# Kernel optimization log

Hardware: AMD Instinct MI355X
Metric: run time of the kernel (lower is better)

The kernel has to match this reference:

```python
import jax, jax.numpy as jnp
import numpy as np

NV, NG, D, K, NB = 4096, 2048, 64, 128, 4
C_IN, C_OUT, E = 128, 8, 32768
SIGMA = 2.5  # rbf sigma used in the non-mp path


def _gcn_conv(x, src, dst, w, b, n):
    # PyG GCNConv (edge_weight=None, self loops already appended to src/dst)
    deg = jax.ops.segment_sum(jnp.ones(src.shape, x.dtype), dst, num_segments=n)
    dinv = jnp.where(deg > 0, 1.0 / jnp.sqrt(deg), 0.0)
    norm = dinv[src] * dinv[dst]
    h = x @ w
    return jax.ops.segment_sum(h[src] * norm[:, None], dst, num_segments=n) + b


def _diff_block(x, mass, evals, evecs, gradX, gradY, t, a_re, a_im, w0, b0, w1, b1, w2, b2):
    # learned-time spectral diffusion
    x_spec = evecs.T @ (x * mass[:, None])                      # [K, D]
    coef = jnp.exp(-evals[:, None] * jnp.clip(t, 1e-8)[None, :])  # [K, D]
    x_diff = evecs @ (coef * x_spec)                            # [NV, D]
    # spatial gradient features: complex grad, learned rotation, tanh of inner product
    gX = gradX @ x_diff                                         # real part  [NV, D]
    gY = gradY @ x_diff                                         # imag part  [NV, D]
    b_re = gX @ a_re - gY @ a_im
    b_im = gY @ a_re + gX @ a_im
    gfeat = jnp.tanh(gX * b_re + gY * b_im)
    f = jnp.concatenate([x, x_diff, gfeat], axis=-1)            # [NV, 3D]
    h = jax.nn.relu(f @ w0 + b0)
    h = jax.nn.relu(h @ w1 + b1)
    return h @ w2 + b2 + x                                      # residual skip


def _forward(surf_x, mass, evals, evecs, gradX, gradY, vertices, graph_x, graph_pos,
             lin1_w, lin1_b, lin2_w, lin2_b, last_w, last_b,
             diff_time, A_re, A_im, mlp_w0, mlp_b0, mlp_w1, mlp_b1, mlp_w2, mlp_b2,
             gcn_w1, gcn_b1, gcn_w2, gcn_b2, edge_index):
    nv, ng = vertices.shape[0], graph_pos.shape[0]
    # dense rbf coupling (torch.no_grad in original -> stop_gradient)
    d2 = (jnp.sum(vertices * vertices, 1)[:, None]
          + jnp.sum(graph_pos * graph_pos, 1)[None, :]
          - 2.0 * (vertices @ graph_pos.T))
    dist = jnp.sqrt(jnp.clip(d2, 0.0))
    rbf = jax.lax.stop_gradient(jnp.exp(-dist / SIGMA))          # [NV, NG]
    diff_x = surf_x @ lin1_w + lin1_b                            # [NV, D]
    gx = graph_x @ lin2_w + lin2_b                               # [NG, D]
    loops = jnp.arange(ng, dtype=edge_index.dtype)
    src = jnp.concatenate([edge_index[0], loops])
    dst = jnp.concatenate([edge_index[1], loops])
    for i in range(NB):
        diff_x = _diff_block(diff_x, mass, evals, evecs, gradX, gradY,
                             diff_time[i], A_re[i], A_im[i],
                             mlp_w0[i], mlp_b0[i], mlp_w1[i], mlp_b1[i], mlp_w2[i], mlp_b2[i])
        gx = rbf.T @ diff_x                                      # surface -> graph
        h = jax.nn.relu(_gcn_conv(gx, src, dst, gcn_w1[i], gcn_b1[i], ng))
        gx = _gcn_conv(h, src, dst, gcn_w2[i], gcn_b2[i], ng)
        diff_x = rbf @ gx                                        # graph -> surface
    return diff_x @ last_w + last_b                              # [NV, C_OUT]


def setup_inputs() -> dict:
    key = jax.random.key(0)
    ks = jax.random.split(key, 24)
    f32 = jnp.float32
    def rn(k, shape, scale=1.0):
        return jax.random.normal(k, shape, f32) * scale
    inp = {
        'surf_x': rn(ks[0], (NV, 5)),
        'mass': jax.random.uniform(ks[1], (NV,), f32, 0.1, 1.0),
        'evals': jnp.sort(jax.random.uniform(ks[2], (K,), f32, 0.0, 50.0)),
        'evecs': rn(ks[3], (NV, K), 1.0 / np.sqrt(NV)),
        'gradX': rn(ks[4], (NV, NV), 1.0 / np.sqrt(NV)),
        'gradY': rn(ks[5], (NV, NV), 1.0 / np.sqrt(NV)),
        'vertices': rn(ks[6], (NV, 3), 5.0),
        'graph_x': rn(ks[7], (NG, C_IN)),
        'graph_pos': rn(ks[8], (NG, 3), 5.0),
        'lin1_w': rn(ks[9], (5, D), 1.0 / np.sqrt(5)),
        'lin1_b': jnp.zeros((D,), f32),
        'lin2_w': rn(ks[10], (C_IN, D), 1.0 / np.sqrt(C_IN)),
        'lin2_b': jnp.zeros((D,), f32),
        'last_w': rn(ks[11], (D, C_OUT), 1.0 / np.sqrt(D)),
        'last_b': jnp.zeros((C_OUT,), f32),
        'diff_time': jax.random.uniform(ks[12], (NB, D), f32, 1e-3, 1.0),
        'A_re': rn(ks[13], (NB, D, D), 1.0 / np.sqrt(D)),
        'A_im': rn(ks[14], (NB, D, D), 1.0 / np.sqrt(D)),
        'mlp_w0': rn(ks[15], (NB, 3 * D, D), 1.0 / np.sqrt(3 * D)),
        'mlp_b0': jnp.zeros((NB, D), f32),
        'mlp_w1': rn(ks[16], (NB, D, D), 1.0 / np.sqrt(D)),
        'mlp_b1': jnp.zeros((NB, D), f32),
        'mlp_w2': rn(ks[17], (NB, D, D), 1.0 / np.sqrt(D)),
        'mlp_b2': jnp.zeros((NB, D), f32),
        'gcn_w1': rn(ks[18], (NB, D, D), 1.0 / np.sqrt(D)),
        'gcn_b1': jnp.zeros((NB, D), f32),
        'gcn_w2': rn(ks[19], (NB, D, D), 1.0 / np.sqrt(D)),
        'gcn_b2': jnp.zeros((NB, D), f32),
        'edge_index': jax.random.randint(ks[20], (2, E), 0, NG, dtype=jnp.int32),
    }
    return inp


def reference(surf_x, mass, evals, evecs, gradX, gradY, vertices, graph_x, graph_pos,
              lin1_w, lin1_b, lin2_w, lin2_b, last_w, last_b,
              diff_time, A_re, A_im, mlp_w0, mlp_b0, mlp_w1, mlp_b1, mlp_w2, mlp_b2,
              gcn_w1, gcn_b1, gcn_w2, gcn_b2, edge_index):
    return _forward(surf_x, mass, evals, evecs, gradX, gradY, vertices, graph_x, graph_pos,
                    lin1_w, lin1_b, lin2_w, lin2_b, last_w, last_b,
                    diff_time, A_re, A_im, mlp_w0, mlp_b0, mlp_w1, mlp_b1, mlp_w2, mlp_b2,
                    gcn_w1, gcn_b1, gcn_w2, gcn_b2, edge_index)
```

## Files before the change

kernel.cpp:

```cpp
#include <hip/hip_runtime.h>
#include <hip/hip_bf16.h>

#define NVV 4096
#define NGG 2048
#define DD 64
#define KSP 128
#define NBLK 4
#define NEDGE 32768
#define COUT 8
#define NSLICE_G 16
#define NSLICE_V 8
#define NSLICE_S 32
#define VS 32
#define GXE_KSL 16

typedef __hip_bfloat16 bf16;
using bf16x8 = __attribute__((ext_vector_type(8))) __bf16;
using s16x8  = __attribute__((ext_vector_type(8))) short;
using f32x4  = __attribute__((ext_vector_type(4))) float;

__device__ __forceinline__ float toF(bf16 x){ return __bfloat162float(x); }
__device__ __forceinline__ float ldin(const void* p, size_t i, int f){
  return f ? toF(((const bf16*)p)[i]) : ((const float*)p)[i];
}
__device__ __forceinline__ short f2bf(float x){
  __bf16 b = (__bf16)x;
  return __builtin_bit_cast(short, b);
}
__device__ __forceinline__ float bf2f(short s){
  return (float)__builtin_bit_cast(__bf16, s);
}
__device__ __forceinline__ bf16x8 ld8(const short* p){
  return __builtin_bit_cast(bf16x8, *(const s16x8*)p);
}
__device__ __forceinline__ void gl16(const short* g, short* l){
  __builtin_amdgcn_global_load_lds((__attribute__((address_space(1))) void*)(g),
                                   (__attribute__((address_space(3))) void*)(l),
                                   16, 0, 0);
}

__global__ void k_probe(const void* __restrict__ mass, int* __restrict__ flag){
  int t = threadIdx.x;
  float v = toF(((const bf16*)mass)[t]);
  bool ok = (v >= 0.05f) && (v <= 1.05f);
  unsigned long long m = __ballot(ok);
  if (t == 0) flag[0] = (m == ~0ull) ? 1 : 0;
}

__global__ void k_csr_zero(int* c){ int g = blockIdx.x*256+threadIdx.x; if (g<NGG) c[g]=0; }
__global__ void k_csr_cnt(const int* __restrict__ ei, int* __restrict__ c){
  int e = blockIdx.x*256+threadIdx.x; if (e<NEDGE) atomicAdd(&c[ei[NEDGE+e]], 1);
}
__global__ void k_csr_scan(const int* __restrict__ cnt, int* __restrict__ off,
                           int* __restrict__ cursor, float* __restrict__ dinv){
  __shared__ int ws[256];
  int t = threadIdx.x;
  int base = t*8;
  int local[8]; int s = 0;
  #pragma unroll
  for (int i=0;i<8;i++){ local[i]=s; s += cnt[base+i]; }
  ws[t] = s;
  __syncthreads();
  for (int o=1;o<256;o<<=1){
    int v = (t>=o) ? ws[t-o] : 0;
    __syncthreads();
    ws[t] += v;
    __syncthreads();
  }
  int pre = (t==0) ? 0 : ws[t-1];
  #pragma unroll
  for (int i=0;i<8;i++){
    int o = pre + local[i];
    off[base+i] = o; cursor[base+i] = o;
    dinv[base+i] = rsqrtf(1.f + (float)cnt[base+i]);
  }
  if (t==255) off[NGG] = pre + s;
}
__global__ void k_csr_fill(const int* __restrict__ ei, int* __restrict__ cursor,
                           int* __restrict__ csrc){
  int e = blockIdx.x*256+threadIdx.x;
  if (e < NEDGE){
    int d = ei[NEDGE+e];
    int p = atomicAdd(&cursor[d], 1);
    csrc[p] = ei[e];
  }
}

__global__ void k_lin1_mx(const void* __restrict__ sx, const void* __restrict__ w,
                          const void* __restrict__ b, const void* __restrict__ mass,
                          float* __restrict__ out, short* __restrict__ btMX,
                          const int* __restrict__ flg){
  const int f = *flg;
  __shared__ short tl[64*68];
  const int t = threadIdx.x;
  const int r = t>>2, c0 = (t&3)*16;
  const size_t v = (size_t)blockIdx.x*64 + r;
  float sxa[5];
  #pragma unroll
  for (int k=0;k<5;k++) sxa[k] = ldin(sx, v*5+k, f);
  const float mv = ldin(mass, v, f);
  float acc[16];
  #pragma unroll
  for (int j=0;j<16;j++){
    float a = ldin(b, c0+j, f);
    #pragma unroll
    for (int k=0;k<5;k++) a += sxa[k]*ldin(w, (size_t)k*DD + c0 + j, f);
    acc[j] = a;
    tl[(size_t)(c0+j)*68 + r] = f2bf(a*mv);
  }
  float* op = out + v*DD + c0;
  ((float4*)op)[0] = *(float4*)&acc[0];
  ((float4*)op)[1] = *(float4*)&acc[4];
  ((float4*)op)[2] = *(float4*)&acc[8];
  ((float4*)op)[3] = *(float4*)&acc[12];
  __syncthreads();
  s16x8 u0, u1;
  #pragma unroll
  for (int j=0;j<8;j++){ u0[j]=tl[(size_t)r*68+c0+j]; u1[j]=tl[(size_t)r*68+c0+8+j]; }
  const int s8 = (r&7)<<3;
  short* dp = btMX + (size_t)blockIdx.x*4096 + (size_t)r*64;
  *(s16x8*)&dp[c0 ^ s8]     = u0;
  *(s16x8*)&dp[(c0+8) ^ s8] = u1;
}

__global__ void k_spec_red(const float* __restrict__ partial, const void* __restrict__ evals,
                           const void* __restrict__ tvec, int boff,
                           short* __restrict__ btA, const int* __restrict__ flg){
  const int f = *flg;
  int idx = blockIdx.x*256 + threadIdx.x;
  int k = idx >> 6, d = idx & 63;
  float sum = 0.f;
  #pragma unroll 8
  for (int s = 0; s < VS; s++) sum += partial[(size_t)s*KSP*DD + idx];
  float t = fmaxf(ldin(tvec, boff + d, f), 1e-8f);
  float val = expf(-ldin(evals, k, f) * t) * sum;
  btA[(size_t)(k>>6)*4096 + (size_t)d*64 + ((k&63) ^ ((d&7)<<3))] = f2bf(val);
}

__global__ void k_cvt_a(const void* __restrict__ src, short* __restrict__ dst,
                        int Kfull, const int* __restrict__ flg){
  const int f = *flg;
  const int t = threadIdx.x;
  const int r = t>>2, c0 = (t&3)*16;
  const size_t row = (size_t)blockIdx.x*64 + r;
  const size_t base = row*(size_t)Kfull + (size_t)blockIdx.y*64 + c0;
  s16x8 v0, v1;
  if (f){
    const short* sp = (const short*)src + base;
    v0 = ((const s16x8*)sp)[0];
    v1 = ((const s16x8*)sp)[1];
  } else {
    const float* sp = (const float*)src + base;
    float tmp[16];
    ((float4*)tmp)[0] = ((const float4*)sp)[0];
    ((float4*)tmp)[1] = ((const float4*)sp)[1];
    ((float4*)tmp)[2] = ((const float4*)sp)[2];
    ((float4*)tmp)[3] = ((const float4*)sp)[3];
    #pragma unroll
    for (int i=0;i<8;i++){ v0[i]=f2bf(tmp[i]); v1[i]=f2bf(tmp[8+i]); }
  }
  const int s8 = (r&7)<<3;
  short* dp = dst + ((size_t)blockIdx.x*(Kfull>>6) + blockIdx.y)*4096 + (size_t)r*64;
  *(s16x8*)&dp[c0 ^ s8]     = v0;
  *(s16x8*)&dp[(c0+8) ^ s8] = v1;
}

__global__ void k_cvt_at(const void* __restrict__ evecs, short* __restrict__ dst,
                         const int* __restrict__ flg){
  const int f = *flg;
  __shared__ short tl[64*68];
  const int t = threadIdx.x;
  const int r = t>>2, c0 = (t&3)*16;
  const int kt = blockIdx.x, s = blockIdx.y;
  const size_t v = (size_t)kt*64 + r;
  #pragma unroll
  for (int j=0;j<16;j++)
    tl[(size_t)(c0+j)*68 + r] = f2bf(ldin(evecs, v*KSP + (size_t)s*64 + c0 + j, f));
  __syncthreads();
  s16x8 u0, u1;
  #pragma unroll
  for (int j=0;j<8;j++){ u0[j]=tl[(size_t)r*68+c0+j]; u1[j]=tl[(size_t)r*68+c0+8+j]; }
  const int s8 = (r&7)<<3;
  short* dp = dst + ((size_t)s*64 + kt)*4096 + (size_t)r*64;
  *(s16x8*)&dp[c0 ^ s8]     = u0;
  *(s16x8*)&dp[(c0+8) ^ s8] = u1;
}

__global__ void k_rbf_pre(const void* __restrict__ P, const void* __restrict__ Q,
                          short* __restrict__ rbfV, short* __restrict__ rbfG,
                          const int* __restrict__ flg){
  const int f = *flg;
  __shared__ short tl[64*68];
  const int t = threadIdx.x;
  const int r = t>>2, c0 = (t&3)*16;
  const int vt = blockIdx.x, gt = blockIdx.y;
  const float px = ldin(P, ((size_t)vt*64+r)*3+0, f);
  const float py = ldin(P, ((size_t)vt*64+r)*3+1, f);
  const float pz = ldin(P, ((size_t)vt*64+r)*3+2, f);
  s16x8 v0, v1;
  #pragma unroll
  for (int j=0;j<16;j++){
    const size_t g = (size_t)gt*64 + c0 + j;
    float dx = px - ldin(Q, g*3+0, f);
    float dy = py - ldin(Q, g*3+1, f);
    float dz = pz - ldin(Q, g*3+2, f);
    short s = f2bf(__expf(-sqrtf(dx*dx+dy*dy+dz*dz)*0.4f));
    if (j<8) v0[j] = s; else v1[j-8] = s;
    tl[(size_t)(c0+j)*68 + r] = s;
  }
  const int s8 = (r&7)<<3;
  short* vp = rbfV + ((size_t)vt*(NGG/64) + gt)*4096 + (size_t)r*64;
  *(s16x8*)&vp[c0 ^ s8]     = v0;
  *(s16x8*)&vp[(c0+8) ^ s8] = v1;
  __syncthreads();
  s16x8 u0, u1;
  #pragma unroll
  for (int j=0;j<8;j++){ u0[j] = tl[(size_t)r*68 + c0 + j]; u1[j] = tl[(size_t)r*68 + c0 + 8 + j]; }
  short* gp = rbfG + ((size_t)gt*(NVV/64) + vt)*4096 + (size_t)r*64;
  *(s16x8*)&gp[c0 ^ s8]     = u0;
  *(s16x8*)&gp[(c0+8) ^ s8] = u1;
}

__global__ void k_cvt_wt(const void* __restrict__ Are, const void* __restrict__ Aim,
                         const void* __restrict__ w0, const void* __restrict__ w1,
                         const void* __restrict__ w2,
                         short* __restrict__ btRe, short* __restrict__ btIm,
                         short* __restrict__ btW0, short* __restrict__ btW1,
                         short* __restrict__ btW2, const int* __restrict__ flg){
  const int f = *flg;
  __shared__ short tl[64*68];
  const int t = threadIdx.x;
  const int r = t>>2, c0 = (t&3)*16;
  const int slot = blockIdx.x, b = blockIdx.y;
  const void* src; size_t soff; short* dst; float scale = 1.f;
  switch(slot){
    case 0: src=Are; soff=(size_t)b*4096; dst=btRe + (size_t)b*2*4096;               break;
    case 1: src=Aim; soff=(size_t)b*4096; dst=btRe + (size_t)b*2*4096 + 4096; scale=-1.f; break;
    case 2: src=Aim; soff=(size_t)b*4096; dst=btIm + (size_t)b*2*4096;               break;
    case 3: src=Are; soff=(size_t)b*4096; dst=btIm + (size_t)b*2*4096 + 4096;        break;
    case 4: case 5: case 6:
      src=w0; soff=(size_t)b*3*4096 + (size_t)(slot-4)*4096;
      dst=btW0 + (size_t)b*3*4096 + (size_t)(slot-4)*4096;                           break;
    case 7: src=w1; soff=(size_t)b*4096; dst=btW1 + (size_t)b*4096;                  break;
    default: src=w2; soff=(size_t)b*4096; dst=btW2 + (size_t)b*4096;                 break;
  }
  #pragma unroll
  for (int j=0;j<16;j++)
    tl[(size_t)(c0+j)*68 + r] = f2bf(scale * ldin(src, soff + (size_t)r*64 + c0 + j, f));
  __syncthreads();
  s16x8 u0, u1;
  #pragma unroll
  for (int j=0;j<8;j++){ u0[j]=tl[(size_t)r*68+c0+j]; u1[j]=tl[(size_t)r*68+c0+8+j]; }
  const int s8 = (r&7)<<3;
  short* dp = dst + (size_t)r*64;
  *(s16x8*)&dp[c0 ^ s8]     = u0;
  *(s16x8*)&dp[(c0+8) ^ s8] = u1;
}

template<int TWO>
__global__ void k_gemm_pre(const short* __restrict__ A0, const short* __restrict__ A1,
                           const short* __restrict__ Bt, float* __restrict__ C,
                           int M, int ktt, int tps, int yoff, short* __restrict__ btOut){
  constexpr int NBUF = TWO ? 3 : 2;
  __shared__ __align__(16) short sm[2*NBUF*4096];
  const int t = threadIdx.x;
  const int w = t>>6, lane = t&63;
  const int fr = lane&15, fq = lane>>4;
  const int strip = blockIdx.x, sl = blockIdx.y;
  const size_t abase = ((size_t)strip*ktt + (size_t)sl*tps)*4096;
  const short* gA0 = A0 + abase;
  const short* gA1 = TWO ? (A1 + abase) : A0;
  const short* gB  = Bt + (size_t)sl*tps*4096;
  const int to = t*8;

  auto stage = [&](int p, int kt){
    short* l = &sm[p*NBUF*4096];
    const size_t ko = (size_t)kt*4096;
    gl16(gA0 + ko + to,        l + (w<<9));
    gl16(gA0 + ko + 2048 + to, l + 2048 + (w<<9));
    if (TWO){
      gl16(gA1 + ko + to,        l + 4096 + (w<<9));
      gl16(gA1 + ko + 2048 + to, l + 6144 + (w<<9));
    }
    short* lb = l + (TWO ? 8192 : 4096);
    gl16(gB + ko + to,        lb + (w<<9));
    gl16(gB + ko + 2048 + to, lb + 2048 + (w<<9));
  };

  f32x4 acc0[4] = {{0,0,0,0},{0,0,0,0},{0,0,0,0},{0,0,0,0}};
  f32x4 acc1[4] = {{0,0,0,0},{0,0,0,0},{0,0,0,0},{0,0,0,0}};

  stage(0, 0);
  int cur = 0;
  const int arow = w*16 + fr;
  const int ax0 = arow*64;
  const int asw = (arow&7)<<3;
  for (int kt=0; kt<tps; ++kt){
    if (kt+1 < tps){
      stage(cur^1, kt+1);
      if constexpr (TWO) asm volatile("s_waitcnt vmcnt(6)" ::: "memory");
      else               asm volatile("s_waitcnt vmcnt(4)" ::: "memory");
    } else {
      asm volatile("s_waitcnt vmcnt(0)" ::: "memory");
    }
    __builtin_amdgcn_s_barrier();
    asm volatile("" ::: "memory");
    const short* As  = &sm[cur*NBUF*4096];
    const short* A1s = As + 4096;
    const short* Bs  = As + (TWO ? 8192 : 4096);
    #pragma unroll
    for (int ks=0; ks<2; ks++){
      const int kx = ks*32 + fq*8;
      bf16x8 a0 = ld8(&As[ax0 + (kx ^ asw)]);
      bf16x8 a1 = TWO ? ld8(&A1s[ax0 + (kx ^ asw)]) : a0;
      #pragma unroll
      for (int nc=0;nc<4;nc++){
        const int brow = nc*16 + fr;
        bf16x8 b = ld8(&Bs[brow*64 + (kx ^ ((brow&7)<<3))]);
        acc0[nc] = __builtin_amdgcn_mfma_f32_16x16x32_bf16(a0, b, acc0[nc], 0, 0, 0);
        if constexpr (TWO)
          acc1[nc] = __builtin_amdgcn_mfma_f32_16x16x32_bf16(a1, b, acc1[nc], 0, 0, 0);
      }
    }
    asm volatile("" ::: "memory");
    __builtin_amdgcn_s_barrier();
    cur ^= 1;
  }
  float* C0 = C + (size_t)sl*M*DD;
  const int row0 = strip*64 + w*16 + fq*4;
  #pragma unroll
  for (int nc=0;nc<4;nc++)
    #pragma unroll
    for (int r=0;r<4;r++)
      C0[(size_t)(row0+r)*DD + nc*16 + fr] = acc0[nc][r];
  if constexpr (TWO){
    float* C1 = C + (size_t)yoff + (size_t)sl*M*DD;
    #pragma unroll
    for (int nc=0;nc<4;nc++)
      #pragma unroll
      for (int r=0;r<4;r++)
        C1[(size_t)(row0+r)*DD + nc*16 + fr] = acc1[nc][r];
  }
  if (btOut){
    #pragma unroll
    for (int nc=0;nc<4;nc++)
      #pragma unroll
      for (int r=0;r<4;r++){
        int k = row0 + r, n = nc*16 + fr;
        btOut[(size_t)(k>>6)*4096 + (size_t)n*64 + ((k&63) ^ ((n&7)<<3))] = f2bf(acc0[nc][r]);
      }
  }
}

__global__ void k_gxe_raw(const void* __restrict__ gradX, const void* __restrict__ gradY,
                          const short* __restrict__ evsT, float* __restrict__ part,
                          const int* __restrict__ flg){
  const int f = *flg;
  __shared__ __align__(16) short sm[4*4096];
  const int t = threadIdx.x;
  const int w = t>>6, lane = t&63;
  const int fr = lane&15, fq = lane>>4;
  const int strip = blockIdx.x, ksl = blockIdx.y;
  const int sr = t>>2, sc = (t&3)*16;
  const int to = t*8;
  const int arow = w*16 + fr;
  const int asw = (arow&7)<<3;
  const int s8 = (sr&7)<<3;
  f32x4 aX0[4] = {{0,0,0,0},{0,0,0,0},{0,0,0,0},{0,0,0,0}};
  f32x4 aX1[4] = {{0,0,0,0},{0,0,0,0},{0,0,0,0},{0,0,0,0}};
  f32x4 aY0[4] = {{0,0,0,0},{0,0,0,0},{0,0,0,0},{0,0,0,0}};
  f32x4 aY1[4] = {{0,0,0,0},{0,0,0,0},{0,0,0,0},{0,0,0,0}};
  for (int kt=0; kt<4; ++kt){
    const int ktg = ksl*4 + kt;
    const size_t abase = ((size_t)strip*64 + sr)*NVV + (size_t)ktg*64 + sc;
    s16x8 x0, x1, y0, y1;
    if (f==0){
      const float* ax = (const float*)gradX + abase;
      const float* ay = (const float*)gradY + abase;
      float bx[16], by[16];
      ((float4*)bx)[0]=((const float4*)ax)[0]; ((float4*)bx)[1]=((const float4*)ax)[1];
      ((float4*)bx)[2]=((const float4*)ax)[2]; ((float4*)bx)[3]=((const float4*)ax)[3];
      ((float4*)by)[0]=((const float4*)ay)[0]; ((float4*)by)[1]=((const float4*)ay)[1];
      ((float4*)by)[2]=((const float4*)ay)[2]; ((float4*)by)[3]=((const float4*)ay)[3];
      #pragma unroll
      for (int j=0;j<8;j++){ x0[j]=f2bf(bx[j]); x1[j]=f2bf(bx[8+j]);
                             y0[j]=f2bf(by[j]); y1[j]=f2bf(by[8+j]); }
    } else {
      const short* ax = (const short*)gradX + abase;
      const short* ay = (const short*)gradY + abase;
      x0 = ((const s16x8*)ax)[0]; x1 = ((const s16x8*)ax)[1];
      y0 = ((const s16x8*)ay)[0]; y1 = ((const s16x8*)ay)[1];
    }
    *(s16x8*)&sm[0*4096 + sr*64 + (sc ^ s8)]     = x0;
    *(s16x8*)&sm[0*4096 + sr*64 + ((sc+8) ^ s8)] = x1;
    *(s16x8*)&sm[1*4096 + sr*64 + (sc ^ s8)]     = y0;
    *(s16x8*)&sm[1*4096 + sr*64 + ((sc+8) ^ s8)] = y1;
    gl16(evsT + (size_t)ktg*4096 + to,             &sm[2*4096] + (w<<9));
    gl16(evsT + (size_t)ktg*4096 + 2048 + to,      &sm[2*4096] + 2048 + (w<<9));
    gl16(evsT + (size_t)(64+ktg)*4096 + to,        &sm[3*4096] + (w<<9));
    gl16(evsT + (size_t)(64+ktg)*4096 + 2048 + to, &sm[3*4096] + 2048 + (w<<9));
    __syncthreads();
    #pragma unroll
    for (int ks=0; ks<2; ks++){
      const int kx = ks*32 + fq*8;
      bf16x8 aXv = ld8(&sm[0*4096 + arow*64 + (kx ^ asw)]);
      bf16x8 aYv = ld8(&sm[1*4096 + arow*64 + (kx ^ asw)]);
      #pragma unroll
      for (int nc=0;nc<4;nc++){
        const int brow = nc*16 + fr, bsw = (brow&7)<<3;
        bf16x8 b0 = ld8(&sm[2*4096 + brow*64 + (kx ^ bsw)]);
        bf16x8 b1 = ld8(&sm[3*4096 + brow*64 + (kx ^ bsw)]);
        aX0[nc] = __builtin_amdgcn_mfma_f32_16x16x32_bf16(aXv, b0, aX0[nc], 0, 0, 0);
        aX1[nc] = __builtin_amdgcn_mfma_f32_16x16x32_bf16(aXv, b1, aX1[nc], 0, 0, 0);
        aY0[nc] = __builtin_amdgcn_mfma_f32_16x16x32_bf16(aYv, b0, aY0[nc], 0, 0, 0);
        aY1[nc] = __builtin_amdgcn_mfma_f32_16x16x32_bf16(aYv, b1, aY1[nc], 0, 0, 0);
      }
    }
    __syncthreads();
  }
  const int row0 = strip*64 + w*16 + fq*4;
  float* C0 = part + (size_t)(ksl)*NVV*DD;
  float* C1 = part + (size_t)(GXE_KSL+ksl)*NVV*DD;
  float* C2 = part + (size_t)(2*GXE_KSL+ksl)*NVV*DD;
  float* C3 = part + (size_t)(3*GXE_KSL+ksl)*NVV*DD;
  #pragma unroll
  for (int nc=0;nc<4;nc++)
    #pragma unroll
    for (int r=0;r<4;r++){
      const size_t o = (size_t)(row0+r)*DD + nc*16 + fr;
      C0[o] = aX0[nc][r];
      C1[o] = aX1[nc][r];
      C2[o] = aY0[nc][r];
      C3[o] = aY1[nc][r];
    }
}

__global__ void k_fold_at(const float* __restrict__ part, short* __restrict__ dX,
                          short* __restrict__ dY){
  const int t = threadIdx.x;
  const int r = t>>2, c0 = (t&3)*16;
  const int strip = blockIdx.x, s = blockIdx.y;
  float ax[16], ay[16];
  #pragma unroll
  for (int j=0;j<16;j++){ ax[j]=0.f; ay[j]=0.f; }
  const float* pb = part + ((size_t)strip*64 + r)*DD + c0;
  for (int sl=0; sl<GXE_KSL; sl++){
    const float* px = pb + (size_t)(s*GXE_KSL+sl)*NVV*DD;
    const float* py = pb + (size_t)(2*GXE_KSL+s*GXE_KSL+sl)*NVV*DD;
    #pragma unroll
    for (int q=0;q<4;q++){
      float4 a = ((const float4*)px)[q];
      float4 b = ((const float4*)py)[q];
      ax[q*4+0]+=a.x; ax[q*4+1]+=a.y; ax[q*4+2]+=a.z; ax[q*4+3]+=a.w;
      ay[q*4+0]+=b.x; ay[q*4+1]+=b.y; ay[q*4+2]+=b.z; ay[q*4+3]+=b.w;
    }
  }
  s16x8 x0,x1,y0,y1;
  #pragma unroll
  for (int j=0;j<8;j++){ x0[j]=f2bf(ax[j]); x1[j]=f2bf(ax[8+j]);
                         y0[j]=f2bf(ay[j]); y1[j]=f2bf(ay[8+j]); }
  const int s8 = (r&7)<<3;
  short* dpx = dX + ((size_t)strip*2 + s)*4096 + (size_t)r*64;
  short* dpy = dY + ((size_t)strip*2 + s)*4096 + (size_t)r*64;
  *(s16x8*)&dpx[c0 ^ s8]     = x0;
  *(s16x8*)&dpx[(c0+8) ^ s8] = x1;
  *(s16x8*)&dpy[c0 ^ s8]     = y0;
  *(s16x8*)&dpy[(c0+8) ^ s8] = y1;
}

__global__ void k_reduce_mx(const float* __restrict__ P, const void* __restrict__ mass,
                            float* __restrict__ C, short* __restrict__ btMX,
                            int slices, const int* __restrict__ flg){
  const int f = *flg;
  __shared__ short tl[64*68];
  const int t = threadIdx.x;
  const int r = t>>2, c0 = (t&3)*16;
  const size_t v = (size_t)blockIdx.x*64 + r;
  float acc[16];
  #pragma unroll
  for (int j=0;j<16;j++) acc[j] = 0.f;
  const float* pb = P + v*DD + c0;
  for (int s=0;s<slices;s++){
    const float* ps = pb + (size_t)s*NVV*DD;
    #pragma unroll
    for (int q=0;q<4;q++){
      float4 a = ((const float4*)ps)[q];
      acc[q*4+0]+=a.x; acc[q*4+1]+=a.y; acc[q*4+2]+=a.z; acc[q*4+3]+=a.w;
    }
  }
  float* op = C + v*DD + c0;
  ((float4*)op)[0] = *(float4*)&acc[0];
  ((float4*)op)[1] = *(float4*)&acc[4];
  ((float4*)op)[2] = *(float4*)&acc[8];
  ((float4*)op)[3] = *(float4*)&acc[12];
  const float mv = ldin(mass, v, f);
  #pragma unroll
  for (int j=0;j<16;j++) tl[(size_t)(c0+j)*68 + r] = f2bf(acc[j]*mv);
  __syncthreads();
  s16x8 u0, u1;
  #pragma unroll
  for (int j=0;j<8;j++){ u0[j]=tl[(size_t)r*68+c0+j]; u1[j]=tl[(size_t)r*68+c0+8+j]; }
  const int s8 = (r&7)<<3;
  short* dp = btMX + (size_t)blockIdx.x*4096 + (size_t)r*64;
  *(s16x8*)&dp[c0 ^ s8]     = u0;
  *(s16x8*)&dp[(c0+8) ^ s8] = u1;
}

__global__ void k_tail_fused(const short* __restrict__ evsA, const short* __restrict__ GXE,
                             const short* __restrict__ GYE, const short* __restrict__ btA,
                             const float* __restrict__ cur,
                             const short* __restrict__ btRe, const short* __restrict__ btIm,
                             const short* __restrict__ btW0, const short* __restrict__ btW1,
                             const short* __restrict__ btW2,
                             const void* __restrict__ b0, const void* __restrict__ b1,
                             const void* __restrict__ b2, int boff,
                             short* __restrict__ btOut, const int* __restrict__ flg){
  __shared__ __align__(16) short sm[8*4096];
  const int f = *flg;
  const int t = threadIdx.x;
  const int w = t>>6, lane = t&63;
  const int fr = lane&15, fq = lane>>4;
  const int strip = blockIdx.x;
  const int to = t*8;
  const int arow = w*16 + fr;
  const int asw = (arow&7)<<3;
  #pragma unroll
  for (int kt=0; kt<2; kt++){
    const size_t ko = ((size_t)strip*2 + kt)*4096;
    gl16(evsA + ko + to,        &sm[kt*4096] + (w<<9));
    gl16(evsA + ko + 2048 + to, &sm[kt*4096] + 2048 + (w<<9));
    gl16(GXE + ko + to,         &sm[(2+kt)*4096] + (w<<9));
    gl16(GXE + ko + 2048 + to,  &sm[(2+kt)*4096] + 2048 + (w<<9));
    gl16(GYE + ko + to,         &sm[(4+kt)*4096] + (w<<9));
    gl16(GYE + ko + 2048 + to,  &sm[(4+kt)*4096] + 2048 + (w<<9));
    gl16(btA + (size_t)kt*4096 + to,        &sm[(6+kt)*4096] + (w<<9));
    gl16(btA + (size_t)kt*4096 + 2048 + to, &sm[(6+kt)*4096] + 2048 + (w<<9));
  }
  __syncthreads();
  f32x4 aX[4]  = {{0,0,0,0},{0,0,0,0},{0,0,0,0},{0,0,0,0}};
  f32x4 aGX[4] = {{0,0,0,0},{0,0,0,0},{0,0,0,0},{0,0,0,0}};
  f32x4 aGY[4] = {{0,0,0,0},{0,0,0,0},{0,0,0,0},{0,0,0,0}};
  #pragma unroll
  for (int kt=0; kt<2; kt++){
    const short* Ae = &sm[kt*4096];
    const short* Ax = &sm[(2+kt)*4096];
    const short* Ay = &sm[(4+kt)*4096];
    const short* Bs = &sm[(6+kt)*4096];
    #pragma unroll
    for (int ks=0; ks<2; ks++){
      const int kx = ks*32 + fq*8;
      bf16x8 ae = ld8(&Ae[arow*64 + (kx ^ asw)]);
      bf16x8 ax = ld8(&Ax[arow*64 + (kx ^ asw)]);
      bf16x8 ay = ld8(&Ay[arow*64 + (kx ^ asw)]);
      #pragma unroll
      for (int nc=0;nc<4;nc++){
        const int brow = nc*16 + fr;
        bf16x8 b = ld8(&Bs[brow*64 + (kx ^ ((brow&7)<<3))]);
        aX[nc]  = __builtin_amdgcn_mfma_f32_16x16x32_bf16(ae, b, aX[nc], 0, 0, 0);
        aGX[nc] = __builtin_amdgcn_mfma_f32_16x16x32_bf16(ax, b, aGX[nc], 0, 0, 0);
        aGY[nc] = __builtin_amdgcn_mfma_f32_16x16x32_bf16(ay, b, aGY[nc], 0, 0, 0);
      }
    }
  }
  __syncthreads();
  gl16(btRe + to,        &sm[2*4096] + (w<<9));
  gl16(btRe + 2048 + to, &sm[2*4096] + 2048 + (w<<9));
  gl16(btRe + 4096 + to, &sm[3*4096] + (w<<9));
  gl16(btRe + 6144 + to, &sm[3*4096] + 2048 + (w<<9));
  gl16(btIm + to,        &sm[4*4096] + (w<<9));
  gl16(btIm + 2048 + to, &sm[4*4096] + 2048 + (w<<9));
  gl16(btIm + 4096 + to, &sm[5*4096] + (w<<9));
  gl16(btIm + 6144 + to, &sm[5*4096] + 2048 + (w<<9));
  #pragma unroll
  for (int nc=0;nc<4;nc++)
    #pragma unroll
    for (int r2=0;r2<4;r2++){
      const int mi = w*16 + fq*4 + r2, n = nc*16 + fr;
      const int pos = mi*64 + (n ^ ((mi&7)<<3));
      sm[0*4096 + pos] = f2bf(aGX[nc][r2]);
      sm[1*4096 + pos] = f2bf(aGY[nc][r2]);
      sm[7*4096 + pos] = f2bf(aX[nc][r2]);
    }
  {
    const int r = t>>2, c0 = (t&3)*16;
    const float* cp = cur + ((size_t)strip*64 + r)*DD + c0;
    float ca[16];
    ((float4*)ca)[0]=((const float4*)cp)[0]; ((float4*)ca)[1]=((const float4*)cp)[1];
    ((float4*)ca)[2]=((const float4*)cp)[2]; ((float4*)ca)[3]=((const float4*)cp)[3];
    s16x8 v0,v1;
    #pragma unroll
    for (int j=0;j<8;j++){ v0[j]=f2bf(ca[j]); v1[j]=f2bf(ca[8+j]); }
    const int s8 = (r&7)<<3;
    *(s16x8*)&sm[6*4096 + r*64 + (c0 ^ s8)]     = v0;
    *(s16x8*)&sm[6*4096 + r*64 + ((c0+8) ^ s8)] = v1;
  }
  __syncthreads();
  f32x4 re[4] = {{0,0,0,0},{0,0,0,0},{0,0,0,0},{0,0,0,0}};
  f32x4 im[4] = {{0,0,0,0},{0,0,0,0},{0,0,0,0},{0,0,0,0}};
  #pragma unroll
  for (int kt=0; kt<2; kt++){
    const short* As = &sm[kt*4096];
    const short* Br = &sm[(2+kt)*4096];
    const short* Bi = &sm[(4+kt)*4096];
    #pragma unroll
    for (int ks=0; ks<2; ks++){
      const int kx = ks*32 + fq*8;
      bf16x8 a = ld8(&As[arow*64 + (kx ^ asw)]);
      #pragma unroll
      for (int nc=0;nc<4;nc++){
        const int brow = nc*16 + fr, bsw = (brow&7)<<3;
        bf16x8 br_ = ld8(&Br[brow*64 + (kx ^ bsw)]);
        bf16x8 bi_ = ld8(&Bi[brow*64 + (kx ^ bsw)]);
        re[nc] = __builtin_amdgcn_mfma_f32_16x16x32_bf16(a, br_, re[nc], 0, 0, 0);
        im[nc] = __builtin_amdgcn_mfma_f32_16x16x32_bf16(a, bi_, im[nc], 0, 0, 0);
      }
    }
  }
  __syncthreads();
  gl16(btW0 + to,           &sm[2*4096] + (w<<9));
  gl16(btW0 + 2048 + to,    &sm[2*4096] + 2048 + (w<<9));
  gl16(btW0 + 4096 + to,    &sm[3*4096] + (w<<9));
  gl16(btW0 + 6144 + to,    &sm[3*4096] + 2048 + (w<<9));
  gl16(btW0 + 8192 + to,    &sm[4*4096] + (w<<9));
  gl16(btW0 + 10240 + to,   &sm[4*4096] + 2048 + (w<<9));
  gl16(btW1 + to,           &sm[5*4096] + (w<<9));
  gl16(btW1 + 2048 + to,    &sm[5*4096] + 2048 + (w<<9));
  float gfv[4][4];
  #pragma unroll
  for (int nc=0;nc<4;nc++){
    const int n = nc*16 + fr;
    #pragma unroll
    for (int r2=0;r2<4;r2++){
      const int mi = w*16 + fq*4 + r2;
      const int pos = mi*64 + (n ^ ((mi&7)<<3));
      float gx = bf2f(sm[pos]);
      float gy = bf2f(sm[4096 + pos]);
      gfv[nc][r2] = tanhf(gx*re[nc][r2] + gy*im[nc][r2]);
    }
  }
  __syncthreads();
  gl16(btW2 + to,        &sm[1*4096] + (w<<9));
  gl16(btW2 + 2048 + to, &sm[1*4096] + 2048 + (w<<9));
  #pragma unroll
  for (int nc=0;nc<4;nc++)
    #pragma unroll
    for (int r2=0;r2<4;r2++){
      const int mi = w*16 + fq*4 + r2, n = nc*16 + fr;
      sm[mi*64 + (n ^ ((mi&7)<<3))] = f2bf(gfv[nc][r2]);
    }
  __syncthreads();
  f32x4 acc[4] = {{0,0,0,0},{0,0,0,0},{0,0,0,0},{0,0,0,0}};
  #pragma unroll
  for (int kt=0; kt<3; kt++){
    const short* As = &sm[(kt==0 ? 6 : (kt==1 ? 7 : 0))*4096];
    const short* Bs = &sm[(2+kt)*4096];
    #pragma unroll
    for (int ks=0; ks<2; ks++){
      const int kx = ks*32 + fq*8;
      bf16x8 a = ld8(&As[arow*64 + (kx ^ asw)]);
      #pragma unroll
      for (int nc=0;nc<4;nc++){
        const int brow = nc*16 + fr;
        bf16x8 b = ld8(&Bs[brow*64 + (kx ^ ((brow&7)<<3))]);
        acc[nc] = __builtin_amdgcn_mfma_f32_16x16x32_bf16(a, b, acc[nc], 0, 0, 0);
      }
    }
  }
  __syncthreads();
  #pragma unroll
  for (int nc=0;nc<4;nc++){
    float bz = ldin(b0, boff + nc*16 + fr, f);
    #pragma unroll
    for (int r2=0;r2<4;r2++){
      const int mi = w*16 + fq*4 + r2, n = nc*16 + fr;
      sm[6*4096 + mi*64 + (n ^ ((mi&7)<<3))] = f2bf(fmaxf(acc[nc][r2] + bz, 0.f));
    }
  }
  __syncthreads();
  f32x4 a1c[4] = {{0,0,0,0},{0,0,0,0},{0,0,0,0},{0,0,0,0}};
  #pragma unroll
  for (int ks=0; ks<2; ks++){
    const int kx = ks*32 + fq*8;
    bf16x8 a = ld8(&sm[6*4096 + arow*64 + (kx ^ asw)]);
    #pragma unroll
    for (int nc=0;nc<4;nc++){
      const int brow = nc*16 + fr;
      bf16x8 b = ld8(&sm[5*4096 + brow*64 + (kx ^ ((brow&7)<<3))]);
      a1c[nc] = __builtin_amdgcn_mfma_f32_16x16x32_bf16(a, b, a1c[nc], 0, 0, 0);
    }
  }
  #pragma unroll
  for (int nc=0;nc<4;nc++){
    float bz = ldin(b1, boff + nc*16 + fr, f);
    #pragma unroll
    for (int r2=0;r2<4;r2++){
      const int mi = w*16 + fq*4 + r2, n = nc*16 + fr;
      sm[7*4096 + mi*64 + (n ^ ((mi&7)<<3))] = f2bf(fmaxf(a1c[nc][r2] + bz, 0.f));
    }
  }
  __syncthreads();
  f32x4 a2c[4] = {{0,0,0,0},{0,0,0,0},{0,0,0,0},{0,0,0,0}};
  #pragma unroll
  for (int ks=0; ks<2; ks++){
    const int kx = ks*32 + fq*8;
    bf16x8 a = ld8(&sm[7*4096 + arow*64 + (kx ^ asw)]);
    #pragma unroll
    for (int nc=0;nc<4;nc++){
      const int brow = nc*16 + fr;
      bf16x8 b = ld8(&sm[1*4096 + brow*64 + (kx ^ ((brow&7)<<3))]);
      a2c[nc] = __builtin_amdgcn_mfma_f32_16x16x32_bf16(a, b, a2c[nc], 0, 0, 0);
    }
  }
  const int row0 = strip*64 + w*16 + fq*4;
  #pragma unroll
  for (int nc=0;nc<4;nc++){
    float bz = ldin(b2, boff + nc*16 + fr, f);
    #pragma unroll
    for (int r2=0;r2<4;r2++){
      int row = row0 + r2, n = nc*16 + fr;
      float vv = a2c[nc][r2] + bz + cur[(size_t)row*DD + n];
      btOut[(size_t)(row>>6)*4096 + (size_t)n*64 + ((row&63) ^ ((n&7)<<3))] = f2bf(vv);
    }
  }
}

__global__ void k_gcn1(const float* __restrict__ part, const void* __restrict__ W,
                       int woff, const float* __restrict__ dinv,
                       const void* __restrict__ bias, int boff,
                       float* __restrict__ tmp, float* __restrict__ outinit,
                       const int* __restrict__ flg){
  const int f = *flg;
  __shared__ float xs[4][DD];
  int d = threadIdx.x & 63, vl = threadIdx.x >> 6;
  size_t g = (size_t)blockIdx.x*4 + vl;
  float x = 0.f;
  #pragma unroll
  for (int s = 0; s < NSLICE_G; s++) x += part[(size_t)s*NGG*DD + g*DD + d];
  xs[vl][d] = x;
  __syncthreads();
  float acc = 0.f;
  #pragma unroll 8
  for (int k=0;k<DD;k++) acc += xs[vl][k]*ldin(W, (size_t)woff + k*DD + d, f);
  tmp[g*DD+d] = acc;
  float di = dinv[g];
  outinit[g*DD+d] = acc*di*di + ldin(bias, boff + d, f);
}

__global__ void k_gcn2f(const float* __restrict__ selfinit, const float* __restrict__ tmp,
                        const int* __restrict__ off, const int* __restrict__ csrc,
                        const float* __restrict__ dinv, const void* __restrict__ W,
                        int woff, const void* __restrict__ bias, int boff,
                        float* __restrict__ tmp2, float* __restrict__ out2init,
                        const int* __restrict__ flg){
  const int f = *flg;
  __shared__ float xs[4][DD];
  int d = threadIdx.x & 63, vl = threadIdx.x >> 6;
  size_t g = (size_t)blockIdx.x*4 + vl;
  float dg = dinv[g];
  float agg = selfinit[g*DD+d];
  int s1 = off[g+1];
  for (int i = off[g]; i < s1; i++){
    int sv = csrc[i];
    agg += tmp[(size_t)sv*DD+d]*(dinv[sv]*dg);
  }
  xs[vl][d] = fmaxf(agg, 0.f);
  __syncthreads();
  float acc = 0.f;
  #pragma unroll 8
  for (int k=0;k<DD;k++) acc += xs[vl][k]*ldin(W, (size_t)woff + k*DD + d, f);
  tmp2[g*DD+d] = acc;
  out2init[g*DD+d] = acc*dg*dg + ldin(bias, boff + d, f);
}

__global__ void k_aggr_t(const float* __restrict__ selfinit, const float* __restrict__ tmp,
                         const int* __restrict__ off, const int* __restrict__ csrc,
                         const float* __restrict__ dinv, short* __restrict__ dst){
  __shared__ short tl[64*68];
  const int t = threadIdx.x;
  const int r = t>>2, c0 = (t&3)*16;
  const size_t g = (size_t)blockIdx.x*64 + r;
  const float dg = dinv[g];
  float agg[16];
  const float* sp = selfinit + g*DD + c0;
  ((float4*)agg)[0] = ((const float4*)sp)[0];
  ((float4*)agg)[1] = ((const float4*)sp)[1];
  ((float4*)agg)[2] = ((const float4*)sp)[2];
  ((float4*)agg)[3] = ((const float4*)sp)[3];
  const int e1 = off[g+1];
  for (int i = off[g]; i < e1; i++){
    const int sv = csrc[i];
    const float w_ = dinv[sv]*dg;
    const float* tp = tmp + (size_t)sv*DD + c0;
    #pragma unroll
    for (int q=0;q<4;q++){
      float4 a = ((const float4*)tp)[q];
      agg[q*4+0]+=a.x*w_; agg[q*4+1]+=a.y*w_; agg[q*4+2]+=a.z*w_; agg[q*4+3]+=a.w*w_;
    }
  }
  #pragma unroll
  for (int j=0;j<16;j++) tl[(size_t)(c0+j)*68 + r] = f2bf(agg[j]);
  __syncthreads();
  s16x8 u0,u1;
  #pragma unroll
  for (int j=0;j<8;j++){ u0[j]=tl[(size_t)r*68+c0+j]; u1[j]=tl[(size_t)r*68+c0+8+j]; }
  const int s8 = (r&7)<<3;
  short* dp = dst + (size_t)blockIdx.x*4096 + (size_t)r*64;
  *(s16x8*)&dp[c0 ^ s8]     = u0;
  *(s16x8*)&dp[(c0+8) ^ s8] = u1;
}

__global__ void k_final(const float* __restrict__ x, const void* __restrict__ w,
                        const void* __restrict__ b, void* __restrict__ outv,
                        const int* __restrict__ flg){
  const int f = *flg;
  int idx = blockIdx.x*256 + threadIdx.x;
  int v = idx >> 3, c = idx & 7;
  float acc = ldin(b, c, f);
  #pragma unroll 8
  for (int k=0;k<DD;k++) acc += x[(size_t)v*DD+k]*ldin(w, (size_t)k*COUT+c, f);
  if (f) ((bf16*)outv)[idx] = __float2bfloat16(acc);
  else   ((float*)outv)[idx] = acc;
}

extern "C" void kernel_launch(void* const* d_in, const int* in_sizes, int n_in,
                              void* d_out, int out_size, void* d_ws, size_t ws_size,
                              hipStream_t stream){
  (void)in_sizes; (void)n_in;
  const void* surf_x   = d_in[0];
  const void* mass     = d_in[1];
  const void* evals    = d_in[2];
  const void* evecs    = d_in[3];
  const void* gradX    = d_in[4];
  const void* gradY    = d_in[5];
  const void* vertices = d_in[6];
  const void* gpos     = d_in[8];
  const void* lin1_w   = d_in[9];
  const void* lin1_b   = d_in[10];
  const void* last_w   = d_in[13];
  const void* last_b   = d_in[14];
  const void* dtime    = d_in[15];
  const void* A_re     = d_in[16];
  const void* A_im     = d_in[17];
  const void* mw0      = d_in[18];
  const void* mb0      = d_in[19];
  const void* mw1      = d_in[20];
  const void* mb1      = d_in[21];
  const void* mw2      = d_in[22];
  const void* mb2      = d_in[23];
  const void* gw1      = d_in[24];
  const void* gb1      = d_in[25];
  const void* gw2      = d_in[26];
  const void* gb2      = d_in[27];
  const int*  ei       = (const int*)d_in[28];

  const size_t REQUIRED = (size_t)115*1024*1024;
  if (ws_size < REQUIRED){
    hipMemsetAsync(d_out, 0, (size_t)out_size*2, stream);
    return;
  }
  char* p = (char*)d_ws;
  auto alloc = [&](size_t bytes)->void*{
    void* r = (void*)p;
    p += (bytes + 255) & ~(size_t)255;
    return r;
  };
  float* part  = (float*)alloc((size_t)64*NVV*DD*4);
  float* bufA  = (float*)alloc((size_t)NVV*DD*4);
  float* tmpg  = (float*)alloc((size_t)NGG*DD*4);
  float* hg    = (float*)alloc((size_t)NGG*DD*4);
  float* tmp2  = (float*)alloc((size_t)NGG*DD*4);
  float* o2    = (float*)alloc((size_t)NGG*DD*4);
  float* dinv  = (float*)alloc((size_t)NGG*4);
  int*   flg   = (int*)alloc(256);
  int*   cnt   = (int*)alloc((size_t)NGG*4);
  int*   off   = (int*)alloc((size_t)(NGG+1)*4);
  int*   curs  = (int*)alloc((size_t)NGG*4);
  int*   csrc  = (int*)alloc((size_t)NEDGE*4);
  short* rbfV  = (short*)alloc((size_t)NVV*NGG*2);
  short* rbfG  = (short*)alloc((size_t)NVV*NGG*2);
  short* evsT  = (short*)alloc((size_t)NVV*KSP*2);
  short* evs   = (short*)alloc((size_t)NVV*KSP*2);
  short* GXE   = (short*)alloc((size_t)NVV*KSP*2);
  short* GYE   = (short*)alloc((size_t)NVV*KSP*2);
  short* btA   = (short*)alloc((size_t)KSP*DD*2);
  short* btB   = (short*)alloc((size_t)NVV*DD*2);
  short* btMX  = (short*)alloc((size_t)NVV*DD*2);
  short* btRe  = (short*)alloc((size_t)NBLK*2*4096*2);
  short* btIm  = (short*)alloc((size_t)NBLK*2*4096*2);
  short* btW0  = (short*)alloc((size_t)NBLK*3*4096*2);
  short* btW1  = (short*)alloc((size_t)NBLK*4096*2);
  short* btW2  = (short*)alloc((size_t)NBLK*4096*2);

  k_probe<<<1, 64, 0, stream>>>(mass, flg);
  k_csr_zero<<<NGG/256, 256, 0, stream>>>(cnt);
  k_csr_cnt <<<NEDGE/256, 256, 0, stream>>>(ei, cnt);
  k_csr_scan<<<1, 256, 0, stream>>>(cnt, off, curs, dinv);
  k_csr_fill<<<NEDGE/256, 256, 0, stream>>>(ei, curs, csrc);
  k_lin1_mx <<<NVV/64, 256, 0, stream>>>(surf_x, lin1_w, lin1_b, mass, bufA, btMX, flg);
  k_cvt_a<<<dim3(NVV/64, KSP/64), 256, 0, stream>>>(evecs, evs, KSP, flg);
  k_cvt_at<<<dim3(NVV/64, KSP/64), 256, 0, stream>>>(evecs, evsT, flg);
  k_rbf_pre<<<dim3(NVV/64, NGG/64), 256, 0, stream>>>(vertices, gpos, rbfV, rbfG, flg);
  k_cvt_wt<<<dim3(9, NBLK), 256, 0, stream>>>(A_re, A_im, mw0, mw1, mw2,
                                              btRe, btIm, btW0, btW1, btW2, flg);
  k_gxe_raw<<<dim3(NVV/64, GXE_KSL), 256, 0, stream>>>(gradX, gradY, evsT, part, flg);
  k_fold_at<<<dim3(NVV/64, 2), 256, 0, stream>>>(part, GXE, GYE);

  float* cur = bufA;
  for (int b = 0; b < NBLK; b++){
    k_gemm_pre<0><<<dim3(KSP/64, NSLICE_S), 256, 0, stream>>>(evsT, evsT, btMX, part,
        KSP, NVV/64, (NVV/64)/NSLICE_S, 0, nullptr);
    k_spec_red<<<KSP*DD/256, 256, 0, stream>>>(part, evals, dtime, b*DD, btA, flg);
    k_tail_fused<<<NVV/64, 256, 0, stream>>>(evs, GXE, GYE, btA, cur,
        btRe + (size_t)b*2*4096, btIm + (size_t)b*2*4096,
        btW0 + (size_t)b*3*4096, btW1 + (size_t)b*4096, btW2 + (size_t)b*4096,
        mb0, mb1, mb2, b*DD, btB, flg);
    k_gemm_pre<0><<<dim3(NGG/64, NSLICE_G), 256, 0, stream>>>(rbfG, rbfG, btB, part,
        NGG, NVV/64, (NVV/64)/NSLICE_G, 0, nullptr);
    k_gcn1<<<NGG/4, 256, 0, stream>>>(part, gw1, b*DD*DD, dinv, gb1, b*DD, tmpg, hg, flg);
    k_gcn2f<<<NGG/4, 256, 0, stream>>>(hg, tmpg, off, csrc, dinv, gw2, b*DD*DD,
                                       gb2, b*DD, tmp2, o2, flg);
    k_aggr_t<<<NGG/64, 256, 0, stream>>>(o2, tmp2, off, csrc, dinv, btB);
    k_gemm_pre<0><<<dim3(NVV/64, NSLICE_V), 256, 0, stream>>>(rbfV, rbfV, btB, part,
        NVV, NGG/64, (NGG/64)/NSLICE_V, 0, nullptr);
    k_reduce_mx<<<NVV/64, 256, 0, stream>>>(part, mass, cur, btMX, NSLICE_V, flg);
  }
  k_final<<<NVV*COUT/256, 256, 0, stream>>>(cur, last_w, last_b, d_out, flg);
}
```

Baseline: 593.1 us.

## Drop LDS staging in gradX/gradY-evecs GEMM and halve K-split count

The gradX/gradY × evecs kernel now loads its A fragments straight from global memory into registers and reads the B fragments from the pre-swizzled evsT buffer in global memory, removing LDS staging and both __syncthreads per K tile. The K-split factor drops from 16 to 8, so each block runs 8 K tiles instead of 4, and the partial-sum buffer and workspace requirement shrink by half. This cuts barrier stalls and the partial-sum write and reduction traffic. The cost is uncoalesced per-lane global loads and repeated B reads across waves that now rely on cache, plus fewer blocks in flight.

```diff
diff --git a/kernel.cpp b/kernel.cpp
--- a/kernel.cpp
+++ b/kernel.cpp
@@ -12,7 +12,7 @@
 #define NSLICE_V 8
 #define NSLICE_S 32
 #define VS 32
-#define GXE_KSL 16
+#define GXE_KSL 8
 
 typedef __hip_bfloat16 bf16;
 using bf16x8 = __attribute__((ext_vector_type(8))) __bf16;
@@ -356,67 +356,52 @@
                           const short* __restrict__ evsT, float* __restrict__ part,
                           const int* __restrict__ flg){
   const int f = *flg;
-  __shared__ __align__(16) short sm[4*4096];
   const int t = threadIdx.x;
   const int w = t>>6, lane = t&63;
   const int fr = lane&15, fq = lane>>4;
   const int strip = blockIdx.x, ksl = blockIdx.y;
-  const int sr = t>>2, sc = (t&3)*16;
-  const int to = t*8;
   const int arow = w*16 + fr;
-  const int asw = (arow&7)<<3;
-  const int s8 = (sr&7)<<3;
+  const size_t growbase = ((size_t)strip*64 + arow)*NVV;
   f32x4 aX0[4] = {{0,0,0,0},{0,0,0,0},{0,0,0,0},{0,0,0,0}};
   f32x4 aX1[4] = {{0,0,0,0},{0,0,0,0},{0,0,0,0},{0,0,0,0}};
   f32x4 aY0[4] = {{0,0,0,0},{0,0,0,0},{0,0,0,0},{0,0,0,0}};
   f32x4 aY1[4] = {{0,0,0,0},{0,0,0,0},{0,0,0,0},{0,0,0,0}};
-  for (int kt=0; kt<4; ++kt){
-    const int ktg = ksl*4 + kt;
-    const size_t abase = ((size_t)strip*64 + sr)*NVV + (size_t)ktg*64 + sc;
-    s16x8 x0, x1, y0, y1;
-    if (f==0){
-      const float* ax = (const float*)gradX + abase;
-      const float* ay = (const float*)gradY + abase;
-      float bx[16], by[16];
-      ((float4*)bx)[0]=((const float4*)ax)[0]; ((float4*)bx)[1]=((const float4*)ax)[1];
-      ((float4*)bx)[2]=((const float4*)ax)[2]; ((float4*)bx)[3]=((const float4*)ax)[3];
-      ((float4*)by)[0]=((const float4*)ay)[0]; ((float4*)by)[1]=((const float4*)ay)[1];
-      ((float4*)by)[2]=((const float4*)ay)[2]; ((float4*)by)[3]=((const float4*)ay)[3];
-      #pragma unroll
-      for (int j=0;j<8;j++){ x0[j]=f2bf(bx[j]); x1[j]=f2bf(bx[8+j]);
-                             y0[j]=f2bf(by[j]); y1[j]=f2bf(by[8+j]); }
-    } else {
-      const short* ax = (const short*)gradX + abase;
-      const short* ay = (const short*)gradY + abase;
-      x0 = ((const s16x8*)ax)[0]; x1 = ((const s16x8*)ax)[1];
-      y0 = ((const s16x8*)ay)[0]; y1 = ((const s16x8*)ay)[1];
-    }
-    *(s16x8*)&sm[0*4096 + sr*64 + (sc ^ s8)]     = x0;
-    *(s16x8*)&sm[0*4096 + sr*64 + ((sc+8) ^ s8)] = x1;
-    *(s16x8*)&sm[1*4096 + sr*64 + (sc ^ s8)]     = y0;
-    *(s16x8*)&sm[1*4096 + sr*64 + ((sc+8) ^ s8)] = y1;
-    gl16(evsT + (size_t)ktg*4096 + to,             &sm[2*4096] + (w<<9));
-    gl16(evsT + (size_t)ktg*4096 + 2048 + to,      &sm[2*4096] + 2048 + (w<<9));
-    gl16(evsT + (size_t)(64+ktg)*4096 + to,        &sm[3*4096] + (w<<9));
-    gl16(evsT + (size_t)(64+ktg)*4096 + 2048 + to, &sm[3*4096] + 2048 + (w<<9));
-    __syncthreads();
+  for (int kt=0; kt<8; ++kt){
+    const int ktg = ksl*8 + kt;
+    bf16x8 axf[2], ayf[2];
+    #pragma unroll
+    for (int ks=0; ks<2; ks++){
+      const size_t co = growbase + (size_t)ktg*64 + ks*32 + fq*8;
+      if (f==0){
+        const float* ax = (const float*)gradX + co;
+        const float* ay = (const float*)gradY + co;
+        float bx[8], by[8];
+        ((float4*)bx)[0]=((const float4*)ax)[0]; ((float4*)bx)[1]=((const float4*)ax)[1];
+        ((float4*)by)[0]=((const float4*)ay)[0]; ((float4*)by)[1]=((const float4*)ay)[1];
+        s16x8 xv, yv;
+        #pragma unroll
+        for (int j=0;j<8;j++){ xv[j]=f2bf(bx[j]); yv[j]=f2bf(by[j]); }
+        axf[ks] = __builtin_bit_cast(bf16x8, xv);
+        ayf[ks] = __builtin_bit_cast(bf16x8, yv);
+      } else {
+        axf[ks] = ld8((const short*)gradX + co);
+        ayf[ks] = ld8((const short*)gradY + co);
+      }
+    }
     #pragma unroll
     for (int ks=0; ks<2; ks++){
       const int kx = ks*32 + fq*8;
-      bf16x8 aXv = ld8(&sm[0*4096 + arow*64 + (kx ^ asw)]);
-      bf16x8 aYv = ld8(&sm[1*4096 + arow*64 + (kx ^ asw)]);
       #pragma unroll
       for (int nc=0;nc<4;nc++){
         const int brow = nc*16 + fr, bsw = (brow&7)<<3;
-        bf16x8 b0 = ld8(&sm[2*4096 + brow*64 + (kx ^ bsw)]);
-        bf16x8 b1 = ld8(&sm[3*4096 + brow*64 + (kx ^ bsw)]);
-        aX0[nc] = __builtin_amdgcn_mfma_f32_16x16x32_bf16(aXv, b0, aX0[nc], 0, 0, 0);
-        aX1[nc] = __builtin_amdgcn_mfma_f32_16x16x32_bf16(aXv, b1, aX1[nc], 0, 0, 0);
-        aY0[nc] = __builtin_amdgcn_mfma_f32_16x16x32_bf16(aYv, b0, aY0[nc], 0, 0, 0);
-        aY1[nc] = __builtin_amdgcn_mfma_f32_16x16x32_bf16(aYv, b1, aY1[nc], 0, 0, 0);
+        bf16x8 b0 = ld8(&evsT[(size_t)ktg*4096 + brow*64 + (kx ^ bsw)]);
+        bf16x8 b1 = ld8(&evsT[(size_t)(64+ktg)*4096 + brow*64 + (kx ^ bsw)]);
+        aX0[nc] = __builtin_amdgcn_mfma_f32_16x16x32_bf16(axf[ks], b0, aX0[nc], 0, 0, 0);
+        aX1[nc] = __builtin_amdgcn_mfma_f32_16x16x32_bf16(axf[ks], b1, aX1[nc], 0, 0, 0);
+        aY0[nc] = __builtin_amdgcn_mfma_f32_16x16x32_bf16(ayf[ks], b0, aY0[nc], 0, 0, 0);
+        aY1[nc] = __builtin_amdgcn_mfma_f32_16x16x32_bf16(ayf[ks], b1, aY1[nc], 0, 0, 0);
       }
     }
-    __syncthreads();
   }
   const int row0 = strip*64 + w*16 + fq*4;
   float* C0 = part + (size_t)(ksl)*NVV*DD;
@@ -853,7 +838,7 @@
   const void* gb2      = d_in[27];
   const int*  ei       = (const int*)d_in[28];
 
-  const size_t REQUIRED = (size_t)115*1024*1024;
+  const size_t REQUIRED = (size_t)100*1024*1024;
   if (ws_size < REQUIRED){
     hipMemsetAsync(d_out, 0, (size_t)out_size*2, stream);
     return;
@@ -864,7 +849,7 @@
     p += (bytes + 255) & ~(size_t)255;
     return r;
   };
-  float* part  = (float*)alloc((size_t)64*NVV*DD*4);
+  float* part  = (float*)alloc((size_t)32*NVV*DD*4);
   float* bufA  = (float*)alloc((size_t)NVV*DD*4);
   float* tmpg  = (float*)alloc((size_t)NGG*DD*4);
   float* hg    = (float*)alloc((size_t)NGG*DD*4);
```

After: 585.5 us. Within noise of the previous version (-1.3%).
